# Kernel tuning notes

Hardware: AMD Instinct MI355X
Metric: run time of the kernel (lower is better)

The kernel has to match this reference:

```python
import jax, jax.numpy as jnp
import numpy as np

D_IN = 1024
D_OUT = 1024
SEQ = 4096


def setup_inputs() -> dict:
    key = jax.random.key(0)
    kx, kq, kk, kv = jax.random.split(key, 4)
    x = jax.random.normal(kx, (SEQ, D_IN), dtype=jnp.float32)
    # torch.rand -> uniform [0,1)
    wquery = jax.random.uniform(kq, (D_IN, D_OUT), dtype=jnp.float32)
    wkey = jax.random.uniform(kk, (D_IN, D_OUT), dtype=jnp.float32)
    wvalue = jax.random.uniform(kv, (D_IN, D_OUT), dtype=jnp.float32)
    return {"x": x, "wquery": wquery, "wkey": wkey, "wvalue": wvalue}


def reference(x, wquery, wkey, wvalue):
    keys = x @ wkey          # [S, d_out]
    queries = x @ wquery     # [S, d_out]
    values = x @ wvalue      # [S, d_out]
    scale = 1.0 / jnp.sqrt(jnp.float32(keys.shape[-1]))
    attn_scores = queries @ keys.T            # [S, S]
    attn_weights = jax.nn.softmax(attn_scores * scale, axis=-1)
    context = attn_weights @ values           # [S, d_out]
    return context
```

## Files before the change

### kernel.cpp

```cpp
#include <hip/hip_runtime.h>
#include <math.h>

#define SEQ 4096
#define DIM 1024

typedef _Float16 f16;
typedef _Float16 f16x8 __attribute__((ext_vector_type(8)));
typedef _Float16 f16x4 __attribute__((ext_vector_type(4)));
typedef float f32x4 __attribute__((ext_vector_type(4)));

#define GLOAD_LDS16(g, l)                                              \
    __builtin_amdgcn_global_load_lds(                                  \
        (const __attribute__((address_space(1))) void*)(g),            \
        (__attribute__((address_space(3))) void*)(l), 16, 0, 0)

__global__ __launch_bounds__(256) void split16rs(const float* __restrict__ in,
                                                 f16* __restrict__ hi,
                                                 f16* __restrict__ lo,
                                                 float* __restrict__ sx) {
    __shared__ float sred[4];
    const int tid = threadIdx.x;
    const int i = blockIdx.x * 256 + tid;
    const float4 v = ((const float4*)in)[i];
    const float vv[4] = {v.x, v.y, v.z, v.w};
    f16x4 h, l;
#pragma unroll
    for (int q = 0; q < 4; ++q) {
        const f16 hq = (f16)vv[q];
        h[q] = hq;
        l[q] = (f16)(vv[q] - (float)hq);
    }
    ((f16x4*)hi)[i] = h;
    ((f16x4*)lo)[i] = l;
    float s = v.x + v.y + v.z + v.w;
#pragma unroll
    for (int m = 32; m >= 1; m >>= 1) s += __shfl_xor(s, m);
    if ((tid & 63) == 0) sred[tid >> 6] = s;
    __syncthreads();
    if (tid == 0) sx[blockIdx.x] = sred[0] + sred[1] + sred[2] + sred[3];
}

__global__ __launch_bounds__(256) void wtrans3h(
    const float* __restrict__ Wq, const float* __restrict__ Wk,
    const float* __restrict__ Wv,
    f16* __restrict__ QT, f16* __restrict__ KT, f16* __restrict__ VT) {
    __shared__ float tile[32][33];
    const int tid = threadIdx.x;
    const int r0 = blockIdx.x * 32;
    const int c0 = blockIdx.y * 32;
    const int z = blockIdx.z;
    const float* W = (z == 0) ? Wq : (z == 1) ? Wk : Wv;
    f16* T = (z == 0) ? QT : (z == 1) ? KT : VT;
    const float off = (z < 2) ? 0.5f : 0.0f;
    {
        const int r = tid >> 3, c = (tid & 7) * 4;
        const float4 v = *(const float4*)&W[(size_t)(r0 + r) * DIM + c0 + c];
        tile[r][c + 0] = v.x;
        tile[r][c + 1] = v.y;
        tile[r][c + 2] = v.z;
        tile[r][c + 3] = v.w;
    }
    __syncthreads();
    {
        const int n = tid >> 3;
        const int k = (tid & 7) * 4;
        f16x4 h;
#pragma unroll
        for (int q = 0; q < 4; ++q) h[q] = (f16)(tile[k + q][n] - off);
        *(f16x4*)&T[(size_t)(c0 + n) * DIM + r0 + k] = h;
    }
}

__global__ __launch_bounds__(256) void rowsum_hl(
    const f16* __restrict__ Qh, const f16* __restrict__ Ql,
    const f16* __restrict__ Kh, const f16* __restrict__ Kl,
    float* __restrict__ rq, float* __restrict__ rk) {
    const f16 *H, *L;
    float* out;
    if (blockIdx.y == 0) { H = Qh; L = Ql; out = rq; }
    else                 { H = Kh; L = Kl; out = rk; }
    const int row = blockIdx.x * 4 + (threadIdx.x >> 6);
    const int lane = threadIdx.x & 63;
    const f16x8* h8 = (const f16x8*)(H + (size_t)row * DIM);
    const f16x8* l8 = (const f16x8*)(L + (size_t)row * DIM);
    float s = 0.f;
#pragma unroll
    for (int c = 0; c < 2; ++c) {
        const f16x8 a = h8[lane + 64 * c];
        const f16x8 b = l8[lane + 64 * c];
#pragma unroll
        for (int e = 0; e < 8; ++e) s += (float)a[e] + (float)b[e];
    }
#pragma unroll
    for (int m = 32; m >= 1; m >>= 1) s += __shfl_xor(s, m);
    if (lane == 0) out[row] = s;
}

#define EPI_F32 0
#define EPI_SPLIT16 1
#define EPI_TRANS16 2

template <int EPI, int NPAIR, int KTILES>
__global__ __launch_bounds__(256, 2) void gemm128h(
    const f16* __restrict__ A0, const f16* __restrict__ A1,
    const f16* __restrict__ B0a, const f16* __restrict__ B1a,
    const f16* __restrict__ B0b, const f16* __restrict__ B1b,
    int ysplit, int N, int ldA, int ldB, float scale,
    void* out0a, void* out1a, void* out0b, void* out1b) {
    __shared__ __align__(16) f16 As[2][128 * 64];
    __shared__ __align__(16) f16 Bs[2][128 * 64];

    const int tid = threadIdx.x;
    const int lane = tid & 63;
    const int wid = tid >> 6;
    const int wr = wid >> 1, wc = wid & 1;

    const int total = (int)(gridDim.y << 5);
    int lid = (int)blockIdx.y * 32 + (int)blockIdx.x;
    lid = (lid & 7) * (total >> 3) + (lid >> 3);
    const int bx = lid & 31;
    int by = lid >> 5;

    const f16 *B0, *B1;
    void *o0, *o1;
    if (by >= ysplit) {
        by -= ysplit;
        B0 = B0b; B1 = B1b;
        o0 = out0b; o1 = out1b;
    } else {
        B0 = B0a; B1 = B1a;
        o0 = out0a; o1 = out1a;
    }
    const int m0 = bx * 128;
    const int n0 = by * 128;

    const f16* APs[2] = {A0, A1};
    const f16* BPs[2] = {B0, B1};
    const int nt = NPAIR * KTILES;

    f32x4 acc[4][4];
#pragma unroll
    for (int i = 0; i < 4; ++i)
#pragma unroll
        for (int j = 0; j < 4; ++j) acc[i][j] = (f32x4){0.f, 0.f, 0.f, 0.f};

    auto STAGE = [&](int t, int b) {
        const int pass = t / KTILES;
        const int k0 = (t % KTILES) * 64;
        const f16* Ap = APs[pass];
        const f16* Bp = BPs[pass];
#pragma unroll
        for (int L = 0; L < 4; ++L) {
            const int idx = L * 256 + tid;
            const int row = idx >> 3;
            const int sc = ((idx & 7) * 16) ^ ((row & 7) << 4);
            const int ldsu = (L * 256 + (tid & ~63)) * 8;
            GLOAD_LDS16(Ap + (size_t)(m0 + row) * ldA + k0 + (sc >> 1),
                        &As[b][ldsu]);
            GLOAD_LDS16(Bp + (size_t)(n0 + row) * ldB + k0 + (sc >> 1),
                        &Bs[b][ldsu]);
        }
    };

    STAGE(0, 0);

    for (int t = 0; t < nt; ++t) {
        const int cur = t & 1;
        __builtin_amdgcn_s_barrier();
        asm volatile("" ::: "memory");
        if (t + 1 < nt) {
            STAGE(t + 1, cur ^ 1);
            asm volatile("s_waitcnt vmcnt(8)" ::: "memory");
        } else {
            asm volatile("s_waitcnt vmcnt(0)" ::: "memory");
        }
        __builtin_amdgcn_s_barrier();
        asm volatile("" ::: "memory");

#pragma unroll
        for (int kk = 0; kk < 2; ++kk) {
            const int cb = kk * 64 + (lane >> 4) * 16;
            f16x8 af[4], bv[4];
#pragma unroll
            for (int i = 0; i < 4; ++i) {
                const int r = wr * 64 + i * 16 + (lane & 15);
                af[i] = *(const f16x8*)(&As[cur][r * 64 +
                                                 ((cb ^ ((r & 7) << 4)) >> 1)]);
            }
#pragma unroll
            for (int j = 0; j < 4; ++j) {
                const int r = wc * 64 + j * 16 + (lane & 15);
                bv[j] = *(const f16x8*)(&Bs[cur][r * 64 +
                                                 ((cb ^ ((r & 7) << 4)) >> 1)]);
            }
            __builtin_amdgcn_s_setprio(1);
#pragma unroll
            for (int i = 0; i < 4; ++i)
#pragma unroll
                for (int j = 0; j < 4; ++j)
                    acc[i][j] = __builtin_amdgcn_mfma_f32_16x16x32_f16(
                        af[i], bv[j], acc[i][j], 0, 0, 0);
            __builtin_amdgcn_s_setprio(0);
        }
    }

    const int row0 = m0 + wr * 64 + (lane >> 4) * 4;
    const int col0 = n0 + wc * 64 + (lane & 15);

    if (EPI == EPI_F32) {
        float* O = (float*)o0;
#pragma unroll
        for (int i = 0; i < 4; ++i)
#pragma unroll
            for (int j = 0; j < 4; ++j)
#pragma unroll
                for (int q = 0; q < 4; ++q)
                    O[(size_t)(row0 + i * 16 + q) * N + col0 + j * 16] =
                        acc[i][j][q] * scale;
    } else if (EPI == EPI_SPLIT16) {
        f16* Hi = (f16*)o0;
        f16* Lo = (f16*)o1;
#pragma unroll
        for (int i = 0; i < 4; ++i)
#pragma unroll
            for (int j = 0; j < 4; ++j)
#pragma unroll
                for (int q = 0; q < 4; ++q) {
                    const float x = acc[i][j][q];
                    const f16 h = (f16)x;
                    const size_t idx = (size_t)(row0 + i * 16 + q) * N + col0 + j * 16;
                    Hi[idx] = h;
                    Lo[idx] = (f16)(x - (float)h);
                }
    } else {
        f16* OT = (f16*)o0;
#pragma unroll
        for (int i = 0; i < 4; ++i)
#pragma unroll
            for (int j = 0; j < 4; ++j) {
                f16x4 v;
#pragma unroll
                for (int q = 0; q < 4; ++q) v[q] = (f16)acc[i][j][q];
                *(f16x4*)&OT[(size_t)(col0 + j * 16) * SEQ + row0 + i * 16] = v;
            }
    }
}

template <int NPAIR, int KT>
__global__ __launch_bounds__(512, 2) void qkrank1(
    const f16* __restrict__ A0, const f16* __restrict__ B0,
    const f16* __restrict__ A1, const f16* __restrict__ B1,
    const float* __restrict__ sx, const float* __restrict__ rq,
    const float* __restrict__ rk,
    f16* __restrict__ Pu, float* __restrict__ Mp, float* __restrict__ Lp) {
    constexpr int K = KT * 64;
    constexpr int nt = NPAIR * KT;
    __shared__ __align__(16) f16 As[2][256 * 64];
    __shared__ __align__(16) f16 Bs[2][256 * 64];

    const int tid = threadIdx.x;
    const int lane = tid & 63;
    const int wid = tid >> 6;
    const int wr = wid >> 2;
    const int wc = wid & 3;

    const int wg = ((int)blockIdx.x & 7) * 32 + ((int)blockIdx.x >> 3);
    const int m0 = (wg >> 4) * 256;
    const int n0 = (wg & 15) * 256;
    const int bcol = n0 >> 8;

    const f16* APs[2] = {A0, A1};
    const f16* BPs[2] = {B0, B1};

    f32x4 acc[8][4];
#pragma unroll
    for (int i = 0; i < 8; ++i)
#pragma unroll
        for (int j = 0; j < 4; ++j) acc[i][j] = (f32x4){0.f, 0.f, 0.f, 0.f};

    auto STAGE = [&](int t, int b) {
        const f16* Ap = APs[t / KT];
        const f16* Bp = BPs[t / KT];
        const int k0 = (t % KT) * 64;
#pragma unroll
        for (int L = 0; L < 4; ++L) {
            const int idx = L * 512 + tid;
            const int row = idx >> 3;
            const int sc = ((idx & 7) * 16) ^ ((row & 7) << 4);
            const int ldsu = (L * 512 + (tid & ~63)) * 8;
            GLOAD_LDS16(Ap + (size_t)(m0 + row) * K + k0 + (sc >> 1),
                        &As[b][ldsu]);
            GLOAD_LDS16(Bp + (size_t)(n0 + row) * K + k0 + (sc >> 1),
                        &Bs[b][ldsu]);
        }
    };

    STAGE(0, 0);

    for (int t = 0; t < nt; ++t) {
        const int cur = t & 1;
        __builtin_amdgcn_s_barrier();
        asm volatile("" ::: "memory");
        if (t + 1 < nt) {
            STAGE(t + 1, cur ^ 1);
            asm volatile("s_waitcnt vmcnt(8)" ::: "memory");
        } else {
            asm volatile("s_waitcnt vmcnt(0)" ::: "memory");
        }
        __builtin_amdgcn_s_barrier();
        asm volatile("" ::: "memory");

#pragma unroll
        for (int kk = 0; kk < 2; ++kk) {
            const int cb = kk * 64 + (lane >> 4) * 16;
            f16x8 af[8], bv[4];
#pragma unroll
            for (int i = 0; i < 8; ++i) {
                const int r = wr * 128 + i * 16 + (lane & 15);
                af[i] = *(const f16x8*)(&As[cur][r * 64 +
                                                 ((cb ^ ((r & 7) << 4)) >> 1)]);
            }
#pragma unroll
            for (int j = 0; j < 4; ++j) {
                const int r = wc * 64 + j * 16 + (lane & 15);
                bv[j] = *(const f16x8*)(&Bs[cur][r * 64 +
                                                 ((cb ^ ((r & 7) << 4)) >> 1)]);
            }
            __builtin_amdgcn_s_setprio(1);
#pragma unroll
            for (int i = 0; i < 8; ++i)
#pragma unroll
                for (int j = 0; j < 4; ++j)
                    acc[i][j] = __builtin_amdgcn_mfma_f32_16x16x32_f16(
                        af[i], bv[j], acc[i][j], 0, 0, 0);
            __builtin_amdgcn_s_setprio(0);
        }
    }

    const int g4 = lane >> 4;
    const int l15 = lane & 15;
    const int row0 = m0 + wr * 128 + g4 * 4;
    const int col0 = n0 + wc * 64 + l15;
    float u[4], w4[4];
#pragma unroll
    for (int j = 0; j < 4; ++j) {
        const float sxc = sx[col0 + j * 16];
        u[j] = 256.f * sxc + 0.5f * rk[col0 + j * 16];
        w4[j] = 0.5f * sxc;
    }
#pragma unroll
    for (int i = 0; i < 8; ++i)
#pragma unroll
        for (int q = 0; q < 4; ++q) {
            const int r = row0 + i * 16 + q;
            const float sxr = sx[r];
            const float rqr = rq[r];
#pragma unroll
            for (int j = 0; j < 4; ++j)
                acc[i][j][q] =
                    (acc[i][j][q] + sxr * u[j] + rqr * w4[j]) * 0.03125f;
        }

    float* partm = (float*)&As[0][0];
    float* mrow  = partm + 1024;
    float* parts = mrow + 256;
    float red[8][4];
#pragma unroll
    for (int i = 0; i < 8; ++i)
#pragma unroll
        for (int q = 0; q < 4; ++q) {
            float v = acc[i][0][q];
#pragma unroll
            for (int j = 1; j < 4; ++j) v = fmaxf(v, acc[i][j][q]);
            red[i][q] = v;
        }
#pragma unroll
    for (int msk = 1; msk < 16; msk <<= 1)
#pragma unroll
        for (int i = 0; i < 8; ++i)
#pragma unroll
            for (int q = 0; q < 4; ++q)
                red[i][q] = fmaxf(red[i][q], __shfl_xor(red[i][q], msk));
    __syncthreads();
    if (l15 == 0)
#pragma unroll
        for (int i = 0; i < 8; ++i)
#pragma unroll
            for (int q = 0; q < 4; ++q)
                partm[(wr * 128 + i * 16 + g4 * 4 + q) * 4 + wc] = red[i][q];
    __syncthreads();
    if (tid < 256) {
        const float* p = partm + tid * 4;
        mrow[tid] = fmaxf(fmaxf(p[0], p[1]), fmaxf(p[2], p[3]));
    }
    __syncthreads();
#pragma unroll
    for (int i = 0; i < 8; ++i)
#pragma unroll
        for (int q = 0; q < 4; ++q) {
            const float mB = mrow[wr * 128 + i * 16 + g4 * 4 + q];
            float s = 0.f;
#pragma unroll
            for (int j = 0; j < 4; ++j) {
                const float e = __expf(acc[i][j][q] - mB);
                acc[i][j][q] = e;
                s += e;
            }
            red[i][q] = s;
        }
#pragma unroll
    for (int msk = 1; msk < 16; msk <<= 1)
#pragma unroll
        for (int i = 0; i < 8; ++i)
#pragma unroll
            for (int q = 0; q < 4; ++q) red[i][q] += __shfl_xor(red[i][q], msk);
    if (l15 == 0)
#pragma unroll
        for (int i = 0; i < 8; ++i)
#pragma unroll
            for (int q = 0; q < 4; ++q)
                parts[(wr * 128 + i * 16 + g4 * 4 + q) * 4 + wc] = red[i][q];
    __syncthreads();
    if (tid < 256) {
        const float* p = parts + tid * 4;
        Mp[(size_t)(m0 + tid) * 16 + bcol] = mrow[tid];
        Lp[(size_t)(m0 + tid) * 16 + bcol] = p[0] + p[1] + p[2] + p[3];
    }
#pragma unroll
    for (int i = 0; i < 8; ++i)
#pragma unroll
        for (int q = 0; q < 4; ++q) {
            const size_t r = row0 + i * 16 + q;
#pragma unroll
            for (int j = 0; j < 4; ++j)
                Pu[r * SEQ + col0 + j * 16] = (f16)acc[i][j][q];
        }
}

__global__ __launch_bounds__(256) void rowfix(const float* __restrict__ Mp,
                                              const float* __restrict__ Lp,
                                              f16* __restrict__ Pu) {
    __shared__ float mls[32];
    const int tid = threadIdx.x;
    const size_t r = blockIdx.x;
    if (tid < 32)
        mls[tid] = (tid < 16) ? Mp[r * 16 + tid] : Lp[r * 16 + tid - 16];
    __syncthreads();
    float m = -1e30f;
#pragma unroll
    for (int b = 0; b < 16; ++b) m = fmaxf(m, mls[b]);
    float l = 0.f;
#pragma unroll
    for (int b = 0; b < 16; ++b) l += __expf(mls[b] - m) * mls[16 + b];
    const float inv = 1.f / l;

    f16* row = Pu + r * SEQ;
#pragma unroll
    for (int p = 0; p < 2; ++p) {
        const int c0 = p * 2048 + tid * 8;
        const float d = __expf(mls[c0 >> 8] - m) * inv;
        f16x8 v = *(const f16x8*)(row + c0);
#pragma unroll
        for (int e = 0; e < 8; ++e) v[e] = (f16)((float)v[e] * d);
        *(f16x8*)(row + c0) = v;
    }
}

extern "C" void kernel_launch(void* const* d_in, const int* in_sizes, int n_in,
                              void* d_out, int out_size, void* d_ws, size_t ws_size,
                              hipStream_t stream) {
    const float* x  = (const float*)d_in[0];
    const float* wq = (const float*)d_in[1];
    const float* wk = (const float*)d_in[2];
    const float* wv = (const float*)d_in[3];
    float* O = (float*)d_out;

    char* ws = (char*)d_ws;
    const size_t MB = 1024 * 1024;
    const size_t KB = 1024;
    f16* Qh = (f16*)(ws + 0 * MB);
    f16* Ql = (f16*)(ws + 8 * MB);
    f16* Kh = (f16*)(ws + 16 * MB);
    f16* VT = (f16*)(ws + 24 * MB);
    float* sx = (float*)(ws + 32 * MB);
    float* rq = (float*)(ws + 32 * MB + 16 * KB);
    float* rk = (float*)(ws + 32 * MB + 32 * KB);
    float* Mp = (float*)(ws + 32 * MB + 48 * KB);
    float* Lp = (float*)(ws + 32 * MB + 304 * KB);
    f16* Pu = (f16*)(ws + 40 * MB);
    f16* Xh  = (f16*)(ws + 40 * MB);
    f16* Xl  = (f16*)(ws + 48 * MB);
    f16* Wqh = (f16*)(ws + 56 * MB);
    f16* Wkh = (f16*)(ws + 58 * MB);
    f16* Wvh = (f16*)(ws + 60 * MB);
    f16* Kl  = (f16*)(ws + 64 * MB);

    split16rs<<<4096, 256, 0, stream>>>(x, Xh, Xl, sx);
    wtrans3h<<<dim3(DIM / 32, DIM / 32, 3), 256, 0, stream>>>(
        wq, wk, wv, Wqh, Wkh, Wvh);

    gemm128h<EPI_SPLIT16, 2, 16><<<dim3(32, 16), 256, 0, stream>>>(
        Xh, Xl, Wqh, Wqh, Wkh, Wkh,
        8, DIM, DIM, DIM, 1.f, Qh, Ql, Kh, Kl);

    rowsum_hl<<<dim3(1024, 2), 256, 0, stream>>>(Qh, Ql, Kh, Kl, rq, rk);

    gemm128h<EPI_TRANS16, 1, 16><<<dim3(32, 8), 256, 0, stream>>>(
        Xh, Xh, Wvh, Wvh, Wvh, Wvh,
        8, DIM, DIM, DIM, 1.f, VT, nullptr, VT, nullptr);

    qkrank1<2, 16><<<256, 512, 0, stream>>>(
        Qh, Kh, Ql, Kh, sx, rq, rk, Pu, Mp, Lp);

    rowfix<<<4096, 256, 0, stream>>>(Mp, Lp, Pu);

    gemm128h<EPI_F32, 1, 64><<<dim3(32, 8), 256, 0, stream>>>(
        Pu, Pu, VT, VT, VT, VT,
        8, DIM, SEQ, SEQ, 1.f, O, nullptr, O, nullptr);
}
```

Baseline: 235.2 us.

## Fuse V projection into QK projection launch and split-K the PV GEMM

The GEMM kernel now takes three operand sets chosen per block row, each with its own epilogue selected at runtime. This lets the Q, K and V projections run in a single launch. The final P·V GEMM is split into two K halves, giving twice as many blocks to fill more CUs, and an extra kernel sums the two fp32 partials. In exchange, V is now computed from both the hi and lo halves of X, which doubles its work. The split-K path also adds 32MB of partial writes plus an add pass, and the runtime epilogue branch may raise register pressure.

```diff
diff --git a/kernel.cpp b/kernel.cpp
--- a/kernel.cpp
+++ b/kernel.cpp
@@ -100,13 +100,18 @@
 #define EPI_SPLIT16 1
 #define EPI_TRANS16 2
 
-template <int EPI, int NPAIR, int KTILES>
-__global__ __launch_bounds__(256, 2) void gemm128h(
-    const f16* __restrict__ A0, const f16* __restrict__ A1,
-    const f16* __restrict__ B0a, const f16* __restrict__ B1a,
-    const f16* __restrict__ B0b, const f16* __restrict__ B1b,
-    int ysplit, int N, int ldA, int ldB, float scale,
-    void* out0a, void* out1a, void* out0b, void* out1b) {
+template <int NPAIR, int KTILES>
+__global__ __launch_bounds__(256, 2) void gemm128s(
+    const f16* __restrict__ A0, const f16* __restrict__ A1, int ldA, int ldB,
+    const f16* __restrict__ B0_0, const f16* __restrict__ B1_0,
+    void* o0_0, void* o1_0,
+    const f16* __restrict__ B0_1, const f16* __restrict__ B1_1,
+    void* o0_1, void* o1_1,
+    const f16* __restrict__ B0_2, const f16* __restrict__ B1_2,
+    void* o0_2, void* o1_2,
+    int aoffPerSet, int boffPerSet,
+    int epi0, int epi1, int epi2,
+    int N, float scale) {
     __shared__ __align__(16) f16 As[2][128 * 64];
     __shared__ __align__(16) f16 Bs[2][128 * 64];
 
@@ -121,16 +126,18 @@
     const int bx = lid & 31;
     int by = lid >> 5;
 
+    const int set = by >> 3;
+    by &= 7;
+
     const f16 *B0, *B1;
     void *o0, *o1;
-    if (by >= ysplit) {
-        by -= ysplit;
-        B0 = B0b; B1 = B1b;
-        o0 = out0b; o1 = out1b;
-    } else {
-        B0 = B0a; B1 = B1a;
-        o0 = out0a; o1 = out1a;
-    }
+    int epi;
+    if (set == 0)      { B0 = B0_0; B1 = B1_0; o0 = o0_0; o1 = o1_0; epi = epi0; }
+    else if (set == 1) { B0 = B0_1; B1 = B1_1; o0 = o0_1; o1 = o1_1; epi = epi1; }
+    else               { B0 = B0_2; B1 = B1_2; o0 = o0_2; o1 = o1_2; epi = epi2; }
+    const int aoff = set * aoffPerSet;
+    const int boff = set * boffPerSet;
+
     const int m0 = bx * 128;
     const int n0 = by * 128;
 
@@ -155,9 +162,9 @@
             const int row = idx >> 3;
             const int sc = ((idx & 7) * 16) ^ ((row & 7) << 4);
             const int ldsu = (L * 256 + (tid & ~63)) * 8;
-            GLOAD_LDS16(Ap + (size_t)(m0 + row) * ldA + k0 + (sc >> 1),
+            GLOAD_LDS16(Ap + (size_t)(m0 + row) * ldA + k0 + (sc >> 1) + aoff,
                         &As[b][ldsu]);
-            GLOAD_LDS16(Bp + (size_t)(n0 + row) * ldB + k0 + (sc >> 1),
+            GLOAD_LDS16(Bp + (size_t)(n0 + row) * ldB + k0 + (sc >> 1) + boff,
                         &Bs[b][ldsu]);
         }
     };
@@ -207,7 +214,7 @@
     const int row0 = m0 + wr * 64 + (lane >> 4) * 4;
     const int col0 = n0 + wc * 64 + (lane & 15);
 
-    if (EPI == EPI_F32) {
+    if (epi == EPI_F32) {
         float* O = (float*)o0;
 #pragma unroll
         for (int i = 0; i < 4; ++i)
@@ -217,7 +224,7 @@
                 for (int q = 0; q < 4; ++q)
                     O[(size_t)(row0 + i * 16 + q) * N + col0 + j * 16] =
                         acc[i][j][q] * scale;
-    } else if (EPI == EPI_SPLIT16) {
+    } else if (epi == EPI_SPLIT16) {
         f16* Hi = (f16*)o0;
         f16* Lo = (f16*)o1;
 #pragma unroll
@@ -464,6 +471,15 @@
         for (int e = 0; e < 8; ++e) v[e] = (f16)((float)v[e] * d);
         *(f16x8*)(row + c0) = v;
     }
+}
+
+__global__ __launch_bounds__(256) void addf(const float* __restrict__ a,
+                                            const float* __restrict__ b,
+                                            float* __restrict__ o) {
+    const int i = blockIdx.x * 256 + threadIdx.x;
+    const float4 x = ((const float4*)a)[i];
+    const float4 y = ((const float4*)b)[i];
+    ((float4*)o)[i] = make_float4(x.x + y.x, x.y + y.y, x.z + y.z, x.w + y.w);
 }
 
 extern "C" void kernel_launch(void* const* d_in, const int* in_sizes, int n_in,
@@ -488,6 +504,8 @@
     float* Mp = (float*)(ws + 32 * MB + 48 * KB);
     float* Lp = (float*)(ws + 32 * MB + 304 * KB);
     f16* Pu = (f16*)(ws + 40 * MB);
+    float* P0 = (float*)(ws + 72 * MB);
+    float* P1 = (float*)(ws + 88 * MB);
     f16* Xh  = (f16*)(ws + 40 * MB);
     f16* Xl  = (f16*)(ws + 48 * MB);
     f16* Wqh = (f16*)(ws + 56 * MB);
@@ -499,22 +517,30 @@
     wtrans3h<<<dim3(DIM / 32, DIM / 32, 3), 256, 0, stream>>>(
         wq, wk, wv, Wqh, Wkh, Wvh);
 
-    gemm128h<EPI_SPLIT16, 2, 16><<<dim3(32, 16), 256, 0, stream>>>(
-        Xh, Xl, Wqh, Wqh, Wkh, Wkh,
-        8, DIM, DIM, DIM, 1.f, Qh, Ql, Kh, Kl);
+    gemm128s<2, 16><<<dim3(32, 24), 256, 0, stream>>>(
+        Xh, Xl, DIM, DIM,
+        Wqh, Wqh, Qh, Ql,
+        Wkh, Wkh, Kh, Kl,
+        Wvh, Wvh, VT, nullptr,
+        0, 0,
+        EPI_SPLIT16, EPI_SPLIT16, EPI_TRANS16,
+        DIM, 1.f);
 
     rowsum_hl<<<dim3(1024, 2), 256, 0, stream>>>(Qh, Ql, Kh, Kl, rq, rk);
-
-    gemm128h<EPI_TRANS16, 1, 16><<<dim3(32, 8), 256, 0, stream>>>(
-        Xh, Xh, Wvh, Wvh, Wvh, Wvh,
-        8, DIM, DIM, DIM, 1.f, VT, nullptr, VT, nullptr);
 
     qkrank1<2, 16><<<256, 512, 0, stream>>>(
         Qh, Kh, Ql, Kh, sx, rq, rk, Pu, Mp, Lp);
 
     rowfix<<<4096, 256, 0, stream>>>(Mp, Lp, Pu);
 
-    gemm128h<EPI_F32, 1, 64><<<dim3(32, 8), 256, 0, stream>>>(
-        Pu, Pu, VT, VT, VT, VT,
-        8, DIM, SEQ, SEQ, 1.f, O, nullptr, O, nullptr);
-}
+    gemm128s<1, 32><<<dim3(32, 16), 256, 0, stream>>>(
+        Pu, Pu, SEQ, SEQ,
+        VT, VT, P0, nullptr,
+        VT, VT, P1, nullptr,
+        VT, VT, P1, nullptr,
+        2048, 2048,
+        EPI_F32, EPI_F32, EPI_F32,
+        DIM, 1.f);
+
+    addf<<<4096, 256, 0, stream>>>(P0, P1, O);
+}
```

New measurement: 227.7 us. 3.2% less time.
